# Kernel optimization log

Hardware: AMD Instinct MI355X
Metric: run time of the kernel (lower is better)

Reference implementation:

```python
import jax, jax.numpy as jnp
import numpy as np

HEAD_DIM = 128
PROJ_DIM = 64


def setup_inputs() -> dict:
    key = jax.random.key(0)
    kq, kk, kv, kr = jax.random.split(key, 4)
    B, H, NQ, NKV = 1, 16, 2048, 4096
    Q = jax.random.normal(kq, (B, H, NQ, HEAD_DIM), dtype=jnp.float32)
    K = jax.random.normal(kk, (B, H, NKV, HEAD_DIM), dtype=jnp.float32)
    V = jax.random.normal(kv, (B, H, NKV, HEAD_DIM), dtype=jnp.float32)
    # R ~ N(0,1) / sqrt(proj_dim), as in the torch __init__
    R = jax.random.normal(kr, (HEAD_DIM, PROJ_DIM), dtype=jnp.float32) / (PROJ_DIM ** 0.5)
    return {"Q": Q, "K": K, "V": V, "R": R}


def reference(Q, K, V, R):
    proj_dim = R.shape[-1]
    scale = 1.0 / (proj_dim ** 0.5)
    # Project Q and K into the random-projection space: [B,H,N,proj_dim]
    Q_proj = jnp.einsum('bhnd,dp->bhnp', Q, R)
    K_proj = jnp.einsum('bhmd,dp->bhmp', K, R)
    # scores: [B,H,NQ,NKV]
    scores = jnp.einsum('bhnp,bhmp->bhnm', Q_proj, K_proj) * scale
    weights = jax.nn.softmax(scores, axis=-1)
    # output: [B,H,NQ,head_dim]
    return jnp.einsum('bhnm,bhmd->bhnd', weights, V)
```

## Files before the change

kernel.cpp:

```cpp
#include <hip/hip_runtime.h>

#define HEADS 16
#define NQ    2048
#define NKV   4096
#define DH    128
#define PDIM  64

typedef __bf16 bf16_t;
typedef bf16_t bf16x8 __attribute__((ext_vector_type(8)));
typedef bf16_t bf16x4 __attribute__((ext_vector_type(4)));
typedef bf16_t bf16x2 __attribute__((ext_vector_type(2)));
typedef float  f32x4  __attribute__((ext_vector_type(4)));
typedef float  f32x16 __attribute__((ext_vector_type(16)));
typedef int    i32x4  __attribute__((ext_vector_type(4)));

typedef __attribute__((address_space(3))) unsigned int       lds_u32;
typedef __attribute__((address_space(1))) const unsigned int glb_u32;

__device__ __forceinline__ void dma16(const void* g, void* l) {
  __builtin_amdgcn_global_load_lds((glb_u32*)g, (lds_u32*)l, 16, 0, 0);
}

__global__ __launch_bounds__(256) void prep_kernel(
    const float* __restrict__ Q, const float* __restrict__ K,
    const float* __restrict__ V, const float* __restrict__ R,
    bf16_t* __restrict__ Qp, bf16_t* __restrict__ Kp, bf16_t* __restrict__ Vt)
{
  __shared__ char lds[32768];
  const int tid = threadIdx.x;
  const int bid = blockIdx.x;

  if (bid >= 1536) {
    float* sF = (float*)lds;
    const int vb = bid - 1536;
    const float* tp = V + (long)vb * 64 * DH;
#pragma unroll
    for (int rep = 0; rep < 8; ++rep) {
      const int slot = tid + rep * 256;
      const int j = slot >> 5, g = slot & 31;
      f32x4 v = *(const f32x4*)(tp + j * DH + g * 4);
      *(f32x4*)(&sF[j * 128 + ((g ^ ((j >> 3) & 7)) << 2)]) = v;
    }
    __syncthreads();

    const int h = vb >> 6, jt = vb & 63;
    bf16_t* op = Vt + (long)h * DH * NKV + jt * 64;
#pragma unroll
    for (int rep = 0; rep < 4; ++rep) {
      const int slot = tid + rep * 256;
      const int d = slot >> 3, j8 = (slot & 7) * 8;
      const int key = slot & 7;
      const int gsw = (((d >> 2) ^ key) << 2) + (d & 3);
      bf16x8 w;
#pragma unroll
      for (int jj = 0; jj < 8; ++jj) w[jj] = (bf16_t)sF[(j8 + jj) * 128 + gsw];
      *(bf16x8*)(op + (long)d * NKV + j8) = w;
    }
    return;
  }

  bf16_t* sR = (bf16_t*)lds;
  bf16_t* sYb = (bf16_t*)(lds + 64 * 136 * 2);

  const int isQ = (bid < 512);
  const float* src = isQ ? Q : K;
  const long row0  = isQ ? (long)bid * 64 : (long)(bid - 512) * 64;
  const float scale = isQ ? 0.18033688011112042f : 1.0f;
  bf16_t* Y = isQ ? Qp : Kp;

#pragma unroll
  for (int rep = 0; rep < 32; ++rep) {
    const int idx = tid + rep * 256;
    sR[(idx & 63) * 136 + (idx >> 6)] = (bf16_t)R[idx];
  }
  __syncthreads();

  const int wave = tid >> 6, lane = tid & 63;
  const int n16  = lane & 15, quad = lane >> 4;

  bf16x8 bfr[4][4];
#pragma unroll
  for (int nt = 0; nt < 4; ++nt)
#pragma unroll
    for (int kk = 0; kk < 4; ++kk)
      bfr[nt][kk] = *(const bf16x8*)(sR + (nt * 16 + n16) * 136 + kk * 32 + quad * 8);

  const int arow = wave * 16 + n16;
  const float* xp = src + (row0 + arow) * DH;
  bf16x8 a[4];
#pragma unroll
  for (int kk = 0; kk < 4; ++kk) {
    const int k0 = kk * 32 + quad * 8;
    f32x4 x0 = *(const f32x4*)(xp + k0);
    f32x4 x1 = *(const f32x4*)(xp + k0 + 4);
    bf16x8 av;
#pragma unroll
    for (int j = 0; j < 4; ++j) { av[j] = (bf16_t)(x0[j] * scale); av[4 + j] = (bf16_t)(x1[j] * scale); }
    a[kk] = av;
  }

  bf16_t* sy = sYb + wave * (16 * 72);
#pragma unroll
  for (int nt = 0; nt < 4; ++nt) {
    f32x4 acc = {0.f, 0.f, 0.f, 0.f};
#pragma unroll
    for (int kk = 0; kk < 4; ++kk)
      acc = __builtin_amdgcn_mfma_f32_16x16x32_bf16(a[kk], bfr[nt][kk], acc, 0, 0, 0);
#pragma unroll
    for (int r = 0; r < 4; ++r)
      sy[(quad * 4 + r) * 72 + nt * 16 + n16] = (bf16_t)acc[r];
  }
  const long xrow = row0 + wave * 16;
  const int row = lane >> 2, cg = lane & 3;
  bf16x8 w0 = *(const bf16x8*)(&sy[row * 72 + cg * 16]);
  bf16x8 w1 = *(const bf16x8*)(&sy[row * 72 + cg * 16 + 8]);
  *(bf16x8*)(Y + (xrow + row) * PDIM + cg * 16)     = w0;
  *(bf16x8*)(Y + (xrow + row) * PDIM + cg * 16 + 8) = w1;
}

__global__ __launch_bounds__(256, 3) void flash_kernel(
    const bf16_t* __restrict__ Qp, const bf16_t* __restrict__ Kp,
    const bf16_t* __restrict__ Vt, bf16_t* __restrict__ Opart,
    float* __restrict__ Lpart, float* __restrict__ Out,
    int splits, int iters)
{
  __shared__ char smem[34816];
  bf16_t* sK = (bf16_t*)smem;
  bf16_t* sV = (bf16_t*)(smem + 8192);

  const int tid  = threadIdx.x;
  const int wave = tid >> 6, lane = tid & 63;
  const int l31  = lane & 31, h = lane >> 5;

  const int head = blockIdx.x & 15;
  const int qt   = (blockIdx.x >> 4) & 15;
  const int sp   = blockIdx.x >> 8;

  const int qbase = qt * 128 + wave * 32;
  const int kv0   = sp * (64 * iters);

  bf16x8 qf[4];
#pragma unroll
  for (int k = 0; k < 4; ++k)
    qf[k] = *(const bf16x8*)(Qp + ((long)head * NQ + qbase + l31) * PDIM
                             + k * 16 + h * 8);

  f32x16 o[4] = {};
  float rsum = 0.f;

  const bf16_t* kpH = Kp + (long)head * NKV * PDIM;
  const bf16_t* vtH = Vt + (long)head * DH * NKV;

  const int sw = ((lane & 7) ^ ((lane >> 3) & 7)) * 8;
  const int r8 = lane >> 3;

  for (int t = 0; t < iters; ++t) {
    const int kvb = kv0 + t * 64;
    __syncthreads();
    if (wave == 0) {
#pragma unroll
      for (int i = 0; i < 6; ++i)
        dma16(kpH + (long)(kvb + i * 8 + r8) * PDIM + sw, smem + i * 1024);
    } else if (wave == 1) {
#pragma unroll
      for (int i = 6; i < 8; ++i)
        dma16(kpH + (long)(kvb + i * 8 + r8) * PDIM + sw, smem + i * 1024);
#pragma unroll
      for (int i = 0; i < 4; ++i)
        dma16(vtH + (long)(i * 8 + r8) * NKV + kvb + sw, smem + 8192 + i * 1024);
    } else if (wave == 2) {
#pragma unroll
      for (int i = 4; i < 10; ++i)
        dma16(vtH + (long)(i * 8 + r8) * NKV + kvb + sw, smem + 8192 + i * 1024);
    } else {
#pragma unroll
      for (int i = 10; i < 16; ++i)
        dma16(vtH + (long)(i * 8 + r8) * NKV + kvb + sw, smem + 8192 + i * 1024);
    }
    __syncthreads();

#pragma unroll
    for (int s = 0; s < 2; ++s) {
      f32x16 sc = {};
      const int r = s * 32 + l31;
#pragma unroll
      for (int k = 0; k < 4; ++k) {
        const int c = 2 * k + h;
        const bf16x8 a = *(const bf16x8*)(sK + r * 64 + ((c ^ (r & 7)) * 8));
        sc = __builtin_amdgcn_mfma_f32_32x32x16_bf16(a, qf[k], sc, 0, 0, 0);
      }
      int pk[4][2];
#pragma unroll
      for (int rg = 0; rg < 4; ++rg) {
        const float p0 = __builtin_amdgcn_exp2f(sc[rg * 4 + 0]);
        const float p1 = __builtin_amdgcn_exp2f(sc[rg * 4 + 1]);
        const float p2 = __builtin_amdgcn_exp2f(sc[rg * 4 + 2]);
        const float p3 = __builtin_amdgcn_exp2f(sc[rg * 4 + 3]);
        rsum += (p0 + p1) + (p2 + p3);
        union { bf16x2 v; int i; } u0, u1;
        u0.v = bf16x2{(bf16_t)p0, (bf16_t)p1};
        u1.v = bf16x2{(bf16_t)p2, (bf16_t)p3};
        pk[rg][0] = u0.i; pk[rg][1] = u1.i;
      }
      int bfr[2][4];
#pragma unroll
      for (int cl = 0; cl < 2; ++cl) {
        const int e00 = __shfl_xor(pk[2 * cl][0], 32);
        const int e01 = __shfl_xor(pk[2 * cl][1], 32);
        const int e10 = __shfl_xor(pk[2 * cl + 1][0], 32);
        const int e11 = __shfl_xor(pk[2 * cl + 1][1], 32);
        bfr[cl][0] = h ? e10 : pk[2 * cl][0];
        bfr[cl][1] = h ? e11 : pk[2 * cl][1];
        bfr[cl][2] = h ? pk[2 * cl + 1][0] : e00;
        bfr[cl][3] = h ? pk[2 * cl + 1][1] : e01;
      }
#pragma unroll
      for (int dsub = 0; dsub < 4; ++dsub) {
        const int rr = dsub * 32 + l31;
#pragma unroll
        for (int cl = 0; cl < 2; ++cl) {
          const int c = 2 * (2 * s + cl) + h;
          const bf16x8 va = *(const bf16x8*)(sV + rr * 64 + ((c ^ (rr & 7)) * 8));
          union { i32x4 i; bf16x8 v; } pb;
          pb.i = i32x4{bfr[cl][0], bfr[cl][1], bfr[cl][2], bfr[cl][3]};
          o[dsub] = __builtin_amdgcn_mfma_f32_32x32x16_bf16(va, pb.v, o[dsub], 0, 0, 0);
        }
      }
    }
  }

  __syncthreads();
  bf16_t* myT = (bf16_t*)(smem + wave * 8704);
  const float lsum = rsum + __shfl_xor(rsum, 32);
  const float scale = (splits > 1) ? 1.0f : (1.0f / lsum);
#pragma unroll
  for (int dsub = 0; dsub < 4; ++dsub)
#pragma unroll
    for (int rg = 0; rg < 4; ++rg) {
      bf16x4 w = { (bf16_t)(o[dsub][rg * 4 + 0] * scale),
                   (bf16_t)(o[dsub][rg * 4 + 1] * scale),
                   (bf16_t)(o[dsub][rg * 4 + 2] * scale),
                   (bf16_t)(o[dsub][rg * 4 + 3] * scale) };
      *(bf16x4*)(myT + l31 * 136 + dsub * 32 + rg * 8 + h * 4) = w;
    }
#pragma unroll
  for (int j = 0; j < 8; ++j) {
    const int ql = j * 4 + (lane >> 4);
    bf16x8 v = *(const bf16x8*)(myT + ql * 136 + (lane & 15) * 8);
    if (splits > 1) {
      *(bf16x8*)(Opart + (((long)sp * HEADS + head) * NQ + qbase + ql) * DH + (lane & 15) * 8) = v;
    } else {
      float* op = Out + ((long)head * NQ + qbase + ql) * DH + (lane & 15) * 8;
      f32x4 a = {(float)v[0], (float)v[1], (float)v[2], (float)v[3]};
      f32x4 b = {(float)v[4], (float)v[5], (float)v[6], (float)v[7]};
      *(f32x4*)op = a; *(f32x4*)(op + 4) = b;
    }
  }
  if (splits > 1 && h == 0)
    Lpart[((long)sp * HEADS + head) * NQ + qbase + l31] = lsum;
}

__global__ __launch_bounds__(256) void combine_kernel(
    const bf16_t* __restrict__ Opart, const float* __restrict__ Lpart,
    float* __restrict__ Out)
{
  const long idx = (long)blockIdx.x * 256 + threadIdx.x;
  const int  d8  = (int)(idx & 15);
  const long hq  = idx >> 4;
  float l = 0.f;
  float acc[8];
#pragma unroll
  for (int j = 0; j < 8; ++j) acc[j] = 0.f;
#pragma unroll
  for (int s = 0; s < 4; ++s) {
    l += Lpart[s * (long)(HEADS * NQ) + hq];
    bf16x8 v = *(const bf16x8*)(Opart + (s * (long)(HEADS * NQ) + hq) * DH + d8 * 8);
#pragma unroll
    for (int j = 0; j < 8; ++j) acc[j] += (float)v[j];
  }
  const float inv = 1.f / l;
  f32x4 o0 = { acc[0] * inv, acc[1] * inv, acc[2] * inv, acc[3] * inv };
  f32x4 o1 = { acc[4] * inv, acc[5] * inv, acc[6] * inv, acc[7] * inv };
  float* op = Out + hq * DH + d8 * 8;
  *(f32x4*)(op)     = o0;
  *(f32x4*)(op + 4) = o1;
}

extern "C" void kernel_launch(void* const* d_in, const int* in_sizes, int n_in,
                              void* d_out, int out_size, void* d_ws, size_t ws_size,
                              hipStream_t stream)
{
  const float* Q = (const float*)d_in[0];
  const float* K = (const float*)d_in[1];
  const float* V = (const float*)d_in[2];
  const float* R = (const float*)d_in[3];
  float* Out = (float*)d_out;

  char* ws = (char*)d_ws;
  bf16_t* Qp = (bf16_t*)(ws);
  bf16_t* Kp = (bf16_t*)(ws + (size_t)(4  << 20));
  bf16_t* Vt = (bf16_t*)(ws + (size_t)(12 << 20));
  bf16_t* Opart = (bf16_t*)(ws + (size_t)(28 << 20));
  float*  Lpart = (float*)(ws + (size_t)(60 << 20));

  const size_t need4 = (size_t)(60 << 20) + 4ull * HEADS * NQ * sizeof(float);
  const int splits = (ws_size >= need4) ? 4 : 1;
  const int iters  = NKV / (64 * splits);

  prep_kernel<<<2560, 256, 0, stream>>>(Q, K, V, R, Qp, Kp, Vt);
  flash_kernel<<<splits * 256, 256, 0, stream>>>(Qp, Kp, Vt, Opart, Lpart, Out,
                                                 splits, iters);
  if (splits == 4)
    combine_kernel<<<2048, 256, 0, stream>>>(Opart, Lpart, Out);
}
```

Before: 189.7 us.

## Replace direct-to-LDS DMA with register-staged prefetch of next KV tile

```diff
diff --git a/kernel.cpp b/kernel.cpp
--- a/kernel.cpp
+++ b/kernel.cpp
@@ -13,13 +13,6 @@
 typedef float  f32x4  __attribute__((ext_vector_type(4)));
 typedef float  f32x16 __attribute__((ext_vector_type(16)));
 typedef int    i32x4  __attribute__((ext_vector_type(4)));
-
-typedef __attribute__((address_space(3))) unsigned int       lds_u32;
-typedef __attribute__((address_space(1))) const unsigned int glb_u32;
-
-__device__ __forceinline__ void dma16(const void* g, void* l) {
-  __builtin_amdgcn_global_load_lds((glb_u32*)g, (lds_u32*)l, 16, 0, 0);
-}
 
 __global__ __launch_bounds__(256) void prep_kernel(
     const float* __restrict__ Q, const float* __restrict__ K,
@@ -127,6 +120,7 @@
   __shared__ char smem[34816];
   bf16_t* sK = (bf16_t*)smem;
   bf16_t* sV = (bf16_t*)(smem + 8192);
+  bf16_t* sB = (bf16_t*)smem;
 
   const int tid  = threadIdx.x;
   const int wave = tid >> 6, lane = tid & 63;
@@ -151,33 +145,36 @@
   const bf16_t* kpH = Kp + (long)head * NKV * PDIM;
   const bf16_t* vtH = Vt + (long)head * DH * NKV;
 
-  const int sw = ((lane & 7) ^ ((lane >> 3) & 7)) * 8;
-  const int r8 = lane >> 3;
+  const int krow = tid >> 3, kc16 = tid & 7;
+  const int lof0 = krow * 64 + ((kc16 ^ (krow & 7)) * 8);
+  i32x4 g0, g1, g2, g3, g4, g5;
+
+#define LOAD_STAGE(KVB)                                                       \
+  {                                                                           \
+    const int kb_ = (KVB);                                                    \
+    g0 = *(const i32x4*)(kpH + (long)(kb_ + krow) * PDIM + kc16 * 8);         \
+    g1 = *(const i32x4*)(kpH + (long)(kb_ + krow + 32) * PDIM + kc16 * 8);    \
+    g2 = *(const i32x4*)(vtH + (long)(krow) * NKV + kb_ + kc16 * 8);          \
+    g3 = *(const i32x4*)(vtH + (long)(krow + 32) * NKV + kb_ + kc16 * 8);     \
+    g4 = *(const i32x4*)(vtH + (long)(krow + 64) * NKV + kb_ + kc16 * 8);     \
+    g5 = *(const i32x4*)(vtH + (long)(krow + 96) * NKV + kb_ + kc16 * 8);     \
+  }
+#define WRITE_STAGE()                                                         \
+  {                                                                           \
+    *(i32x4*)(sB + lof0)         = g0;                                        \
+    *(i32x4*)(sB + lof0 + 2048)  = g1;                                        \
+    *(i32x4*)(sB + lof0 + 4096)  = g2;                                        \
+    *(i32x4*)(sB + lof0 + 6144)  = g3;                                        \
+    *(i32x4*)(sB + lof0 + 8192)  = g4;                                        \
+    *(i32x4*)(sB + lof0 + 10240) = g5;                                        \
+  }
+
+  LOAD_STAGE(kv0);
+  WRITE_STAGE();
+  __syncthreads();
 
   for (int t = 0; t < iters; ++t) {
-    const int kvb = kv0 + t * 64;
-    __syncthreads();
-    if (wave == 0) {
-#pragma unroll
-      for (int i = 0; i < 6; ++i)
-        dma16(kpH + (long)(kvb + i * 8 + r8) * PDIM + sw, smem + i * 1024);
-    } else if (wave == 1) {
-#pragma unroll
-      for (int i = 6; i < 8; ++i)
-        dma16(kpH + (long)(kvb + i * 8 + r8) * PDIM + sw, smem + i * 1024);
-#pragma unroll
-      for (int i = 0; i < 4; ++i)
-        dma16(vtH + (long)(i * 8 + r8) * NKV + kvb + sw, smem + 8192 + i * 1024);
-    } else if (wave == 2) {
-#pragma unroll
-      for (int i = 4; i < 10; ++i)
-        dma16(vtH + (long)(i * 8 + r8) * NKV + kvb + sw, smem + 8192 + i * 1024);
-    } else {
-#pragma unroll
-      for (int i = 10; i < 16; ++i)
-        dma16(vtH + (long)(i * 8 + r8) * NKV + kvb + sw, smem + 8192 + i * 1024);
-    }
-    __syncthreads();
+    if (t + 1 < iters) LOAD_STAGE(kv0 + (t + 1) * 64);
 
 #pragma unroll
     for (int s = 0; s < 2; ++s) {
@@ -227,6 +224,10 @@
         }
       }
     }
+
+    __syncthreads();
+    if (t + 1 < iters) WRITE_STAGE();
+    __syncthreads();
   }
 
   __syncthreads();
```

After: 194.7 us. 1.03x slower.

## Double-buffer K/V tiles in LDS to overlap DMA with MFMA compute

Applied to the files above, without the earlier changes.

```diff
diff --git a/kernel.cpp b/kernel.cpp
--- a/kernel.cpp
+++ b/kernel.cpp
@@ -124,9 +124,7 @@
     float* __restrict__ Lpart, float* __restrict__ Out,
     int splits, int iters)
 {
-  __shared__ char smem[34816];
-  bf16_t* sK = (bf16_t*)smem;
-  bf16_t* sV = (bf16_t*)(smem + 8192);
+  __shared__ char smem[49152];
 
   const int tid  = threadIdx.x;
   const int wave = tid >> 6, lane = tid & 63;
@@ -154,30 +152,47 @@
   const int sw = ((lane & 7) ^ ((lane >> 3) & 7)) * 8;
   const int r8 = lane >> 3;
 
+#define STAGE(BASE, KVB)                                                      \
+  {                                                                           \
+    const int kb_ = (KVB);                                                    \
+    char* b_ = (BASE);                                                        \
+    if (wave == 0) {                                                          \
+      _Pragma("unroll")                                                       \
+      for (int i = 0; i < 6; ++i)                                             \
+        dma16(kpH + (long)(kb_ + i * 8 + r8) * PDIM + sw, b_ + i * 1024);     \
+    } else if (wave == 1) {                                                   \
+      _Pragma("unroll")                                                       \
+      for (int i = 6; i < 8; ++i)                                             \
+        dma16(kpH + (long)(kb_ + i * 8 + r8) * PDIM + sw, b_ + i * 1024);     \
+      _Pragma("unroll")                                                       \
+      for (int i = 0; i < 4; ++i)                                             \
+        dma16(vtH + (long)(i * 8 + r8) * NKV + kb_ + sw,                      \
+              b_ + 8192 + i * 1024);                                          \
+    } else if (wave == 2) {                                                   \
+      _Pragma("unroll")                                                       \
+      for (int i = 4; i < 10; ++i)                                            \
+        dma16(vtH + (long)(i * 8 + r8) * NKV + kb_ + sw,                      \
+              b_ + 8192 + i * 1024);                                          \
+    } else {                                                                  \
+      _Pragma("unroll")                                                       \
+      for (int i = 10; i < 16; ++i)                                           \
+        dma16(vtH + (long)(i * 8 + r8) * NKV + kb_ + sw,                      \
+              b_ + 8192 + i * 1024);                                          \
+    }                                                                         \
+  }
+
+  STAGE(smem, kv0);
+  asm volatile("s_waitcnt vmcnt(0)" ::: "memory");
+  __builtin_amdgcn_s_barrier();
+  __builtin_amdgcn_sched_barrier(0);
+
   for (int t = 0; t < iters; ++t) {
-    const int kvb = kv0 + t * 64;
-    __syncthreads();
-    if (wave == 0) {
-#pragma unroll
-      for (int i = 0; i < 6; ++i)
-        dma16(kpH + (long)(kvb + i * 8 + r8) * PDIM + sw, smem + i * 1024);
-    } else if (wave == 1) {
-#pragma unroll
-      for (int i = 6; i < 8; ++i)
-        dma16(kpH + (long)(kvb + i * 8 + r8) * PDIM + sw, smem + i * 1024);
-#pragma unroll
-      for (int i = 0; i < 4; ++i)
-        dma16(vtH + (long)(i * 8 + r8) * NKV + kvb + sw, smem + 8192 + i * 1024);
-    } else if (wave == 2) {
-#pragma unroll
-      for (int i = 4; i < 10; ++i)
-        dma16(vtH + (long)(i * 8 + r8) * NKV + kvb + sw, smem + 8192 + i * 1024);
-    } else {
-#pragma unroll
-      for (int i = 10; i < 16; ++i)
-        dma16(vtH + (long)(i * 8 + r8) * NKV + kvb + sw, smem + 8192 + i * 1024);
-    }
-    __syncthreads();
+    char* cur = smem + ((t & 1) ? 24576 : 0);
+    if (t + 1 < iters)
+      STAGE(smem + ((t & 1) ? 0 : 24576), kv0 + (t + 1) * 64);
+
+    bf16_t* sK = (bf16_t*)cur;
+    bf16_t* sV = (bf16_t*)(cur + 8192);
 
 #pragma unroll
     for (int s = 0; s < 2; ++s) {
@@ -227,6 +242,10 @@
         }
       }
     }
+
+    asm volatile("s_waitcnt vmcnt(0)" ::: "memory");
+    __builtin_amdgcn_s_barrier();
+    __builtin_amdgcn_sched_barrier(0);
   }
 
   __syncthreads();
@@ -258,6 +277,7 @@
   }
   if (splits > 1 && h == 0)
     Lpart[((long)sp * HEADS + head) * NQ + qbase + l31] = lsum;
+#undef STAGE
 }
 
 __global__ __launch_bounds__(256) void combine_kernel(
```

New measurement: 190.2 us. No clear change (+0.2%).
